# Performance work log

Hardware: AMD Instinct MI355X
Metric: run time of the kernel (lower is better)

The kernel has to match this reference:

```python
import jax, jax.numpy as jnp
import numpy as np

EPS = 1e-10

def setup_inputs() -> dict:
    key = jax.random.key(0)
    k1, k2 = jax.random.split(key)
    B, N, D = 8, 4096, 3
    points_ref = jax.random.normal(k1, (B, N, D), dtype=jnp.float32)
    points = jax.random.normal(k2, (B, N, D), dtype=jnp.float32)
    return {"points_ref": points_ref, "points": points, "nn_size": 16}

def _knn(points_ref, K):
    # pairwise squared distances (B,N,N)
    sq = jnp.sum(points_ref * points_ref, axis=-1)
    d2 = sq[:, :, None] + sq[:, None, :] - 2.0 * jnp.einsum('bnd,bmd->bnm', points_ref, points_ref)
    _, idx = jax.lax.top_k(-d2, K)  # nearest first; idx: (B,N,K)
    return idx

def reference(points_ref, points, nn_size):
    K = nn_size + 1
    knn_idx = _knn(points_ref, K)[:, :, 1:]  # drop self -> (B,N,nn_size)
    gather = jax.vmap(lambda p, i: p[i])  # (N,D),(N,K) -> (N,K,D)
    group_ref = gather(points_ref, knn_idx)           # (B,N,K,D)
    group_pred = gather(points, knn_idx)              # (B,N,K,D)
    dist_ref = jnp.linalg.norm(group_ref - points_ref[:, :, None, :], axis=-1)  # (B,N,K)
    dist = jnp.linalg.norm(group_pred - points[:, :, None, :], axis=-1)         # (B,N,K)
    stretch = jnp.maximum(dist / (dist_ref + EPS) - 1.0, 0.0)
    return jnp.mean(stretch)
```

## Files before the change

kernel.cpp:

```cpp
#include <hip/hip_runtime.h>

#define NPTS  4096
#define KNN   16
#define K1    17
#define NBLK  64
#define CELLS 4096
#define EPSF  1e-10f

__device__ __forceinline__ unsigned umin_(unsigned a, unsigned b) { return a < b ? a : b; }
__device__ __forceinline__ unsigned umax_(unsigned a, unsigned b) { return a < b ? b : a; }
__device__ __forceinline__ unsigned rdlane(unsigned v, int l) {
    return (unsigned)__builtin_amdgcn_readlane((int)v, l);
}

#define DPP_XOR1(v)  ((unsigned)__builtin_amdgcn_update_dpp(0, (int)(v), 0xB1, 0xF, 0xF, true))
#define DPP_XOR2(v)  ((unsigned)__builtin_amdgcn_update_dpp(0, (int)(v), 0x4E, 0xF, 0xF, true))
#define SWZ_XOR(v,J) ((unsigned)__builtin_amdgcn_ds_swizzle((int)(v), ((J) << 10) | 0x1F))
#define DPP_SHR1(v)  ((unsigned)__builtin_amdgcn_update_dpp(0, (int)(v), 0x111, 0xF, 0xF, true))
#define DPPF_SHR(vf, CTRL) __uint_as_float((unsigned)__builtin_amdgcn_update_dpp(0, (int)__float_as_uint(vf), CTRL, 0xF, 0xF, true))
#define LXOR1(v)  DPP_XOR1(v)
#define LXOR2(v)  DPP_XOR2(v)
#define LXOR4(v)  SWZ_XOR(v, 4)
#define LXOR8(v)  SWZ_XOR(v, 8)
#define LXOR16(v) SWZ_XOR(v, 16)
#define LXOR32(v) ((unsigned)__shfl_xor((int)(v), 32))

#define BSTEP(K, XORF) do {                                                   \
    unsigned o1_ = XORF(arr), o2_ = XORF(bk);                                 \
    bool tm_ = (((lane & (J_)) == 0) == ((lane & (K)) == 0));                 \
    unsigned mn1_ = umin_(arr, o1_), mx1_ = umax_(arr, o1_);                  \
    unsigned mn2_ = umin_(bk, o2_),  mx2_ = umax_(bk, o2_);                   \
    arr = tm_ ? mn1_ : mx1_; bk = tm_ ? mn2_ : mx2_;                          \
} while (0)

__device__ __forceinline__ unsigned sp4(int v) {
    unsigned x = (unsigned)v;
    return (x & 1u) | ((x & 2u) << 2) | ((x & 4u) << 4) | ((x & 8u) << 6);
}

__global__ __launch_bounds__(1024) void sort_kernel(
    const float* __restrict__ pref,
    float4* __restrict__ wxyzw, int* __restrict__ widx)
{
    __shared__ unsigned hist[CELLS];
    __shared__ unsigned short cells[NPTS];
    __shared__ unsigned wofs[16];
    const int tid  = threadIdx.x;
    const int lane = tid & 63, w = tid >> 6;
    const int b = blockIdx.x;
    const float* prb = pref + (size_t)b * NPTS * 3;
    const size_t base = (size_t)b * NPTS;

    for (int t = tid; t < CELLS; t += 1024) hist[t] = 0u;
    __syncthreads();

    for (int p = tid; p < NPTS; p += 1024) {
        float x = prb[3 * p + 0], y = prb[3 * p + 1], z = prb[3 * p + 2];
        int cx = min(15, max(0, (int)((x + 4.0f) * 2.0f)));
        int cy = min(15, max(0, (int)((y + 4.0f) * 2.0f)));
        int cz = min(15, max(0, (int)((z + 4.0f) * 2.0f)));
        unsigned m = sp4(cx) | (sp4(cy) << 1) | (sp4(cz) << 2);
        cells[p] = (unsigned short)m;
        atomicAdd(&hist[m], 1u);
    }
    __syncthreads();

    unsigned l0 = hist[4 * tid + 0], l1 = hist[4 * tid + 1];
    unsigned l2 = hist[4 * tid + 2], l3 = hist[4 * tid + 3];
    unsigned s = l0 + l1 + l2 + l3;
    unsigned run = s;
#pragma unroll
    for (int d = 1; d < 64; d <<= 1) {
        unsigned o = __shfl_up(run, d);
        if (lane >= d) run += o;
    }
    if (lane == 63) wofs[w] = run;
    __syncthreads();
    if (tid == 0) {
        unsigned acc = 0;
#pragma unroll
        for (int k = 0; k < 16; ++k) { unsigned t2 = wofs[k]; wofs[k] = acc; acc += t2; }
    }
    __syncthreads();
    unsigned excl = wofs[w] + run - s;
    hist[4 * tid + 0] = excl;
    hist[4 * tid + 1] = excl + l0;
    hist[4 * tid + 2] = excl + l0 + l1;
    hist[4 * tid + 3] = excl + l0 + l1 + l2;
    __syncthreads();

    for (int p = tid; p < NPTS; p += 1024) {
        unsigned c = cells[p];
        unsigned pos = atomicAdd(&hist[c], 1u);
        wxyzw[base + pos] = make_float4(prb[3 * p + 0], prb[3 * p + 1], prb[3 * p + 2], 0.f);
        widx[base + pos]  = p;
    }
}

__global__ __launch_bounds__(512) void bbox_kernel(
    const float4* __restrict__ wxyzw, float4* __restrict__ wbb)
{
    const int lane = threadIdx.x & 63;
    const int gb = blockIdx.x * 8 + (threadIdx.x >> 6);
    const int b  = gb >> 6;
    const int blk = gb & (NBLK - 1);
    const size_t base = (size_t)b * NPTS;

    float4 c = wxyzw[base + blk * 64 + lane];
    float mnx = c.x, mxx = c.x, mny = c.y, mxy2 = c.y, mnz = c.z, mxz = c.z;
#pragma unroll
    for (int d = 32; d > 0; d >>= 1) {
        mnx  = fminf(mnx,  __shfl_xor(mnx,  d));
        mxx  = fmaxf(mxx,  __shfl_xor(mxx,  d));
        mny  = fminf(mny,  __shfl_xor(mny,  d));
        mxy2 = fmaxf(mxy2, __shfl_xor(mxy2, d));
        mnz  = fminf(mnz,  __shfl_xor(mnz,  d));
        mxz  = fmaxf(mxz,  __shfl_xor(mxz,  d));
    }
    if (lane == 0) {
        wbb[(size_t)gb * 2 + 0] = make_float4(mnx, mny, mnz, 0.f);
        wbb[(size_t)gb * 2 + 1] = make_float4(mxx, mxy2, mxz, 0.f);
    }
}

#define EVENTS(KEY) do {                                                      \
    unsigned long long m_ = __ballot((KEY) < thr);                            \
    if (m_) {                                                                 \
        do {                                                                  \
            int l_ = __ffsll(m_) - 1;                                         \
            m_ &= m_ - 1;                                                     \
            unsigned kk_ = rdlane(KEY, l_);                                   \
            unsigned long long lt_ = __ballot(arr < kk_) & 0x1FFFFull;        \
            int pos_ = __popcll(lt_);                                         \
            unsigned up_ = DPP_SHR1(arr);                                     \
            unsigned a15_ = rdlane(arr, 15);                                  \
            up_ = (lane == 16) ? a15_ : up_;                                  \
            arr = (lane == pos_) ? kk_ : ((lane > pos_) ? up_ : arr);         \
        } while (m_);                                                         \
        thr = rdlane(arr, K1 - 1);                                            \
    } } while (0)

__global__ __launch_bounds__(256, 8) void knn_main_kernel(
    const float* __restrict__ ppred,
    const float4* __restrict__ wxyzw, const int* __restrict__ widx,
    const float4* __restrict__ wbb, float* __restrict__ partials, int NQ)
{
    __shared__ float wsum[4];
    const int lane = threadIdx.x & 63;
    const int w    = threadIdx.x >> 6;
    const int wv   = blockIdx.x * 4 + w;
    const int q = ((NQ & (NQ - 1)) == 0) ? (int)(((unsigned)wv * 26765u) & (unsigned)(NQ - 1)) : wv;

    const int b = q >> 12;
    const int p = q & (NPTS - 1);
    const size_t base = (size_t)b * NPTS;
    const int p0 = p & ~63, ownblk = p >> 6;

    const float4 qc = wxyzw[base + p];
    const float qx = qc.x, qy = qc.y, qz = qc.z;

    unsigned arr;
    {
        float4 c = wxyzw[base + p0 + lane];
        float dx = c.x - qx, dy = c.y - qy, dz = c.z - qz;
        float d2 = dx * dx + dy * dy + dz * dz;
        arr = (__float_as_uint(d2) & 0xFFFFF000u) | (unsigned)(p0 + lane);
    }
    unsigned bk;
    {
        float4 mn4 = wbb[((size_t)b * NBLK + lane) * 2 + 0];
        float4 mx4 = wbb[((size_t)b * NBLK + lane) * 2 + 1];
        float ddx = fmaxf(fmaxf(mn4.x - qx, qx - mx4.x), 0.0f);
        float ddy = fmaxf(fmaxf(mn4.y - qy, qy - mx4.y), 0.0f);
        float ddz = fmaxf(fmaxf(mn4.z - qz, qz - mx4.z), 0.0f);
        float bd2 = ddx * ddx + ddy * ddy + ddz * ddz;
        bk = (__float_as_uint(bd2) & 0xFFFFF000u) | (unsigned)lane;
        bk = (lane == ownblk) ? 0xFFFFFFFFu : bk;
    }

    {
        int J_;
        J_ = 1;  BSTEP(2,  LXOR1);
        J_ = 2;  BSTEP(4,  LXOR2);  J_ = 1; BSTEP(4,  LXOR1);
        J_ = 4;  BSTEP(8,  LXOR4);  J_ = 2; BSTEP(8,  LXOR2);  J_ = 1; BSTEP(8,  LXOR1);
        J_ = 8;  BSTEP(16, LXOR8);  J_ = 4; BSTEP(16, LXOR4);  J_ = 2; BSTEP(16, LXOR2);  J_ = 1; BSTEP(16, LXOR1);
        J_ = 16; BSTEP(32, LXOR16); J_ = 8; BSTEP(32, LXOR8);  J_ = 4; BSTEP(32, LXOR4);  J_ = 2; BSTEP(32, LXOR2); J_ = 1; BSTEP(32, LXOR1);
        J_ = 32; BSTEP(64, LXOR32); J_ = 16; BSTEP(64, LXOR16); J_ = 8; BSTEP(64, LXOR8); J_ = 4; BSTEP(64, LXOR4); J_ = 2; BSTEP(64, LXOR2); J_ = 1; BSTEP(64, LXOR1);
    }
    unsigned thr = rdlane(arr, K1 - 1);

    int k = 0;
    unsigned bcur = rdlane(bk, 0);
    bool have = (bcur < thr);
    float4 cur;
    if (have) cur = wxyzw[base + (int)(bcur & 0xFFFu) * 64 + lane];
    while (have) {
        unsigned bnext = rdlane(bk, k + 1);
        bool pf = (bnext < thr);
        float4 nxt;
        if (pf) nxt = wxyzw[base + (int)(bnext & 0xFFFu) * 64 + lane];
        int jbase = (int)(bcur & 0xFFFu) * 64;
        float dx = cur.x - qx, dy = cur.y - qy, dz = cur.z - qz;
        float d2 = dx * dx + dy * dy + dz * dz;
        unsigned key = (__float_as_uint(d2) & 0xFFFFF000u) | (unsigned)(jbase + lane);
        EVENTS(key);
        ++k;
        bcur = bnext;
        have = (bcur < thr);
        cur = nxt;
    }

    const float* ppb = ppred + (size_t)b * NPTS * 3;
    const int iorig = widx[base + p];
    float s = 0.f;
    if (lane >= 1 && lane <= KNN) {
        int js = (int)(arr & 0xFFFu);
        float4 rc = wxyzw[base + js];
        float rx = rc.x - qx, ry = rc.y - qy, rz = rc.z - qz;
        float dref = sqrtf(rx * rx + ry * ry + rz * rz);
        int nj = widx[base + js];
        float px = ppb[3 * iorig + 0], py = ppb[3 * iorig + 1], pz = ppb[3 * iorig + 2];
        float ax = ppb[3 * nj + 0] - px;
        float ay = ppb[3 * nj + 1] - py;
        float az = ppb[3 * nj + 2] - pz;
        float dpred = sqrtf(ax * ax + ay * ay + az * az);
        s = fmaxf(dpred / (dref + EPSF) - 1.0f, 0.0f);
    }
    s += DPPF_SHR(s, 0x111);
    s += DPPF_SHR(s, 0x112);
    s += DPPF_SHR(s, 0x114);
    s += DPPF_SHR(s, 0x118);
    float t15 = __uint_as_float(rdlane(__float_as_uint(s), 15));
    float t16 = __uint_as_float(rdlane(__float_as_uint(s), 16));

    if (lane == 0) wsum[w] = t15 + t16;
    __syncthreads();
    if (threadIdx.x == 0)
        partials[blockIdx.x] = (wsum[0] + wsum[1]) + (wsum[2] + wsum[3]);
}

__global__ __launch_bounds__(1024) void reduce_kernel(
    const float* __restrict__ partials, int n, float* __restrict__ out, float scale)
{
    __shared__ float wsum[16];
    const float4* p4 = (const float4*)partials;
    const int n4 = n >> 2;
    float s = 0.f;
    for (int idx = threadIdx.x; idx < n4; idx += 1024) {
        float4 v = p4[idx];
        s += (v.x + v.y) + (v.z + v.w);
    }
    for (int off = 32; off > 0; off >>= 1) s += __shfl_down(s, off);
    if ((threadIdx.x & 63) == 0) wsum[threadIdx.x >> 6] = s;
    __syncthreads();
    if (threadIdx.x == 0) {
        float t = 0.f;
#pragma unroll
        for (int k = 0; k < 16; ++k) t += wsum[k];
        out[0] = t * scale;
    }
}

extern "C" void kernel_launch(void* const* d_in, const int* in_sizes, int n_in,
                              void* d_out, int out_size, void* d_ws, size_t ws_size,
                              hipStream_t stream) {
    const float* pref  = (const float*)d_in[0];
    const float* ppred = (const float*)d_in[1];
    float* out = (float*)d_out;

    const int B  = in_sizes[0] / (NPTS * 3);
    const int NQ = B * NPTS;
    const int nblocks = NQ / 4;
    const float scale = 1.0f / ((float)NQ * (float)KNN);

    char* ws = (char*)d_ws;
    float4* wxyzw = (float4*)ws;
    int*    widx  = (int*)   (ws + (size_t)B * NPTS * 16);
    float4* wbb   = (float4*)(ws + (size_t)B * NPTS * 20);
    float*  partials = (float*)(ws + (size_t)B * NPTS * 20 + (size_t)B * NBLK * 32);

    sort_kernel<<<dim3(B), dim3(1024), 0, stream>>>(pref, wxyzw, widx);
    bbox_kernel<<<dim3(B * NBLK / 8), dim3(512), 0, stream>>>(wxyzw, wbb);
    knn_main_kernel<<<dim3(nblocks), dim3(256), 0, stream>>>(ppred, wxyzw, widx, wbb, partials, NQ);
    reduce_kernel<<<dim3(1), dim3(1024), 0, stream>>>(partials, nblocks, out, scale);
}
```

Baseline: 65.64 us.

## Split per-batch counting sort into histogram, scan and scatter kernels

The single-block-per-batch sort kernel is replaced by a memset plus three kernels. A 64-block histogram pass uses global atomics, a per-batch scan follows, and a 64-block scatter pass writes sorted points and indices. The aim is to spread the sort across more CUs instead of 8 blocks. In exchange it adds launch overhead, global-memory atomics instead of LDS ones, and extra workspace traffic for the cell ids and histograms.

New measurement: 70.04 us. +6.7%, slower.

```diff
diff --git a/kernel.cpp b/kernel.cpp
--- a/kernel.cpp
+++ b/kernel.cpp
@@ -38,35 +38,31 @@
     return (x & 1u) | ((x & 2u) << 2) | ((x & 4u) << 4) | ((x & 8u) << 6);
 }
 
-__global__ __launch_bounds__(1024) void sort_kernel(
-    const float* __restrict__ pref,
-    float4* __restrict__ wxyzw, int* __restrict__ widx)
-{
-    __shared__ unsigned hist[CELLS];
-    __shared__ unsigned short cells[NPTS];
+__global__ __launch_bounds__(512) void hist_kernel(
+    const float* __restrict__ pref, unsigned short* __restrict__ cells,
+    unsigned* __restrict__ hist)
+{
+    const int b = blockIdx.x >> 3;
+    const int p = (blockIdx.x & 7) * 512 + threadIdx.x;
+    const float* prb = pref + (size_t)b * NPTS * 3;
+    float x = prb[3 * p + 0], y = prb[3 * p + 1], z = prb[3 * p + 2];
+    int cx = min(15, max(0, (int)((x + 4.0f) * 2.0f)));
+    int cy = min(15, max(0, (int)((y + 4.0f) * 2.0f)));
+    int cz = min(15, max(0, (int)((z + 4.0f) * 2.0f)));
+    unsigned m = sp4(cx) | (sp4(cy) << 1) | (sp4(cz) << 2);
+    cells[(size_t)b * NPTS + p] = (unsigned short)m;
+    atomicAdd(&hist[(size_t)b * CELLS + m], 1u);
+}
+
+__global__ __launch_bounds__(1024) void scan_kernel(unsigned* __restrict__ hist)
+{
     __shared__ unsigned wofs[16];
     const int tid  = threadIdx.x;
     const int lane = tid & 63, w = tid >> 6;
-    const int b = blockIdx.x;
-    const float* prb = pref + (size_t)b * NPTS * 3;
-    const size_t base = (size_t)b * NPTS;
-
-    for (int t = tid; t < CELLS; t += 1024) hist[t] = 0u;
-    __syncthreads();
-
-    for (int p = tid; p < NPTS; p += 1024) {
-        float x = prb[3 * p + 0], y = prb[3 * p + 1], z = prb[3 * p + 2];
-        int cx = min(15, max(0, (int)((x + 4.0f) * 2.0f)));
-        int cy = min(15, max(0, (int)((y + 4.0f) * 2.0f)));
-        int cz = min(15, max(0, (int)((z + 4.0f) * 2.0f)));
-        unsigned m = sp4(cx) | (sp4(cy) << 1) | (sp4(cz) << 2);
-        cells[p] = (unsigned short)m;
-        atomicAdd(&hist[m], 1u);
-    }
-    __syncthreads();
-
-    unsigned l0 = hist[4 * tid + 0], l1 = hist[4 * tid + 1];
-    unsigned l2 = hist[4 * tid + 2], l3 = hist[4 * tid + 3];
+    unsigned* hb = hist + (size_t)blockIdx.x * CELLS;
+
+    unsigned l0 = hb[4 * tid + 0], l1 = hb[4 * tid + 1];
+    unsigned l2 = hb[4 * tid + 2], l3 = hb[4 * tid + 3];
     unsigned s = l0 + l1 + l2 + l3;
     unsigned run = s;
 #pragma unroll
@@ -83,18 +79,24 @@
     }
     __syncthreads();
     unsigned excl = wofs[w] + run - s;
-    hist[4 * tid + 0] = excl;
-    hist[4 * tid + 1] = excl + l0;
-    hist[4 * tid + 2] = excl + l0 + l1;
-    hist[4 * tid + 3] = excl + l0 + l1 + l2;
-    __syncthreads();
-
-    for (int p = tid; p < NPTS; p += 1024) {
-        unsigned c = cells[p];
-        unsigned pos = atomicAdd(&hist[c], 1u);
-        wxyzw[base + pos] = make_float4(prb[3 * p + 0], prb[3 * p + 1], prb[3 * p + 2], 0.f);
-        widx[base + pos]  = p;
-    }
+    hb[4 * tid + 0] = excl;
+    hb[4 * tid + 1] = excl + l0;
+    hb[4 * tid + 2] = excl + l0 + l1;
+    hb[4 * tid + 3] = excl + l0 + l1 + l2;
+}
+
+__global__ __launch_bounds__(512) void scatter_kernel(
+    const float* __restrict__ pref, const unsigned short* __restrict__ cells,
+    unsigned* __restrict__ hist, float4* __restrict__ wxyzw, int* __restrict__ widx)
+{
+    const int b = blockIdx.x >> 3;
+    const int p = (blockIdx.x & 7) * 512 + threadIdx.x;
+    const size_t base = (size_t)b * NPTS;
+    const float* prb = pref + (size_t)b * NPTS * 3;
+    unsigned c = cells[base + p];
+    unsigned pos = atomicAdd(&hist[(size_t)b * CELLS + c], 1u);
+    wxyzw[base + pos] = make_float4(prb[3 * p + 0], prb[3 * p + 1], prb[3 * p + 2], 0.f);
+    widx[base + pos]  = p;
 }
 
 __global__ __launch_bounds__(512) void bbox_kernel(
@@ -274,12 +276,18 @@
     const float scale = 1.0f / ((float)NQ * (float)KNN);
 
     char* ws = (char*)d_ws;
-    float4* wxyzw = (float4*)ws;
-    int*    widx  = (int*)   (ws + (size_t)B * NPTS * 16);
-    float4* wbb   = (float4*)(ws + (size_t)B * NPTS * 20);
-    float*  partials = (float*)(ws + (size_t)B * NPTS * 20 + (size_t)B * NBLK * 32);
-
-    sort_kernel<<<dim3(B), dim3(1024), 0, stream>>>(pref, wxyzw, widx);
+    size_t off = 0;
+    float4* wxyzw = (float4*)(ws + off);           off += (size_t)B * NPTS * 16;
+    int*    widx  = (int*)   (ws + off);           off += (size_t)B * NPTS * 4;
+    float4* wbb   = (float4*)(ws + off);           off += (size_t)B * NBLK * 32;
+    float*  partials = (float*)(ws + off);         off += (size_t)nblocks * 4;
+    unsigned short* cells = (unsigned short*)(ws + off); off += (size_t)B * NPTS * 2;
+    unsigned* hist = (unsigned*)(ws + off);
+
+    hipMemsetAsync(hist, 0, (size_t)B * CELLS * sizeof(unsigned), stream);
+    hist_kernel<<<dim3(B * 8), dim3(512), 0, stream>>>(pref, cells, hist);
+    scan_kernel<<<dim3(B), dim3(1024), 0, stream>>>(hist);
+    scatter_kernel<<<dim3(B * 8), dim3(512), 0, stream>>>(pref, cells, hist, wxyzw, widx);
     bbox_kernel<<<dim3(B * NBLK / 8), dim3(512), 0, stream>>>(wxyzw, wbb);
     knn_main_kernel<<<dim3(nblocks), dim3(256), 0, stream>>>(ppred, wxyzw, widx, wbb, partials, NQ);
     reduce_kernel<<<dim3(1), dim3(1024), 0, stream>>>(partials, nblocks, out, scale);
```
